# Kernel optimization log

Measured on AMD Instinct MI355X. Metric: run time of the kernel, lower is better.

## Reference

```python
import jax, jax.numpy as jnp
import numpy as np

HEAD_DIM = 64
N_HEADS = 12
ROPE_BASE = 10000.0


def _rope_tables(seq_len, head_dim, dtype=jnp.float32):
    half = head_dim // 2
    inv_freq = 1.0 / (ROPE_BASE ** (jnp.arange(0, half, dtype=jnp.float32) / half))
    pos = jnp.arange(seq_len, dtype=jnp.float32)
    freqs = pos[:, None] * inv_freq[None, :]  # (s, half)
    return jnp.cos(freqs).astype(dtype), jnp.sin(freqs).astype(dtype)


def _apply_rope(t, cos, sin):
    # t: (b, h, s, d); rotate-half convention on full head_dim (rope_fraction=1.0)
    d = t.shape[-1]
    t1, t2 = t[..., : d // 2], t[..., d // 2 :]
    cos = cos[None, None, :, :]
    sin = sin[None, None, :, :]
    return jnp.concatenate([t1 * cos - t2 * sin, t1 * sin + t2 * cos], axis=-1)


def setup_inputs() -> dict:
    key = jax.random.key(0)
    ks = jax.random.split(key, 6)
    b, s, d_model = 16, 512, 768
    x = jax.random.normal(ks[0], (b, s, d_model), dtype=jnp.float32)
    chain_ids = jax.random.randint(ks[1], (b, s), 0, 2, dtype=jnp.int32)
    attention_mask = jnp.ones((b, s), dtype=bool)
    inner = N_HEADS * HEAD_DIM
    scale = 0.02
    Wq = jax.random.normal(ks[2], (d_model, inner), dtype=jnp.float32) * scale
    Wk = jax.random.normal(ks[3], (d_model, inner), dtype=jnp.float32) * scale
    Wv = jax.random.normal(ks[4], (d_model, inner), dtype=jnp.float32) * scale
    Wo = jax.random.normal(ks[5], (inner, d_model), dtype=jnp.float32) * scale
    return {"x": x, "chain_ids": chain_ids, "attention_mask": attention_mask,
            "Wq": Wq, "Wk": Wk, "Wv": Wv, "Wo": Wo}


def reference(x, chain_ids, attention_mask, Wq, Wk, Wv, Wo):
    b, s, _ = x.shape
    h, d = N_HEADS, HEAD_DIM
    scale = d ** (-0.5)

    def proj(W):
        return jnp.einsum('bse,ef->bsf', x, W).reshape(b, s, h, d).transpose(0, 2, 1, 3)

    q = proj(Wq)  # (b, h, s, d)
    k = proj(Wk)
    v = proj(Wv)

    cos, sin = _rope_tables(s, d, x.dtype)
    q_rope = _apply_rope(q, cos, sin)
    k_rope = _apply_rope(k, cos, sin)

    scores_intra = jnp.einsum('bhsd,bhtd->bhst', q_rope, k_rope) * scale
    scores_inter = jnp.einsum('bhsd,bhtd->bhst', q, k) * scale

    # intra-chain mask (b, 1, s, s)
    intra = (chain_ids[:, None, :, None] == chain_ids[:, None, None, :])
    merged = jnp.where(intra, scores_intra, scores_inter)

    # additive padding mask (b, 1, 1, s)
    pad = jnp.where(attention_mask[:, None, None, :], 0.0, -jnp.inf).astype(x.dtype)
    merged = merged + pad

    attn = jax.nn.softmax(merged, axis=-1)
    attn = jnp.nan_to_num(attn, nan=0.0)

    out = jnp.einsum('bhst,bhtd->bhsd', attn, v)
    out = out.transpose(0, 2, 1, 3).reshape(b, s, h * d)
    return jnp.einsum('bsf,fe->bse', out, Wo)
```

## Files before the change

kernel.cpp:

```cpp
#include <hip/hip_runtime.h>
#include <stdint.h>
#include <math.h>

#define NB 16
#define NS 512
#define NH 12
#define ND 64
#define NE 768
#define NF 768

typedef __attribute__((ext_vector_type(4))) float  f32x4;
typedef __attribute__((ext_vector_type(8))) short  bf16x8;
typedef __attribute__((ext_vector_type(4))) short  bf16x4;

#define AS1(p) ((const __attribute__((address_space(1))) unsigned int*)(p))
#define AS3(p) ((__attribute__((address_space(3))) unsigned int*)(p))

__device__ __forceinline__ short f2bf(float f) {
    unsigned u = __builtin_bit_cast(unsigned, f);
    u += 0x7FFFu + ((u >> 16) & 1u);
    return (short)(u >> 16);
}
__device__ __forceinline__ float bf2f(short s) {
    unsigned u = ((unsigned)(unsigned short)s) << 16;
    return __builtin_bit_cast(float, u);
}
__device__ __forceinline__ unsigned pkbf2(float a, float b) {
    return (unsigned)(unsigned short)f2bf(a) | ((unsigned)(unsigned short)f2bf(b) << 16);
}

#define MFMA16(a, b, c) __builtin_amdgcn_mfma_f32_16x16x32_bf16((a), (b), (c), 0, 0, 0)

__device__ __forceinline__ bf16x8 lds_rd8(const short* base, int row, int cb) {
    return *(const bf16x8*)((const char*)base + (((row) * 128 + (cb)) ^ (((row) & 7) << 4)));
}

__global__ __launch_bounds__(256) void prep_kernel(float* __restrict__ cos_t,
                                                   float* __restrict__ sin_t,
                                                   const unsigned char* __restrict__ m,
                                                   int* __restrict__ flag) {
    if (blockIdx.x == 64) {
        __shared__ int any;
        if (threadIdx.x == 0) any = 0;
        __syncthreads();
        int acc = 0;
        for (int i = threadIdx.x; i < NB * NS; i += 256)
            if ((i & 3) && m[i]) acc = 1;
        if (acc) atomicOr(&any, 1);
        __syncthreads();
        if (threadIdx.x == 0) *flag = any;
        return;
    }
    int i = blockIdx.x * 256 + threadIdx.x;
    int p = i >> 5, j = i & 31;
    float inv_freq = powf(10000.0f, -(float)j / 32.0f);
    float ang = (float)p * inv_freq;
    cos_t[i] = cosf(ang);
    sin_t[i] = sinf(ang);
}

__global__ __launch_bounds__(256) void convert_x_kernel(const float* __restrict__ x,
                                                        short* __restrict__ xb) {
    int i = (blockIdx.x * 256 + threadIdx.x) * 8;
    if (i >= 8192 * 768) return;
    float4 a = *(const float4*)&x[i];
    float4 b = *(const float4*)&x[i + 4];
    bf16x8 r = { f2bf(a.x), f2bf(a.y), f2bf(a.z), f2bf(a.w),
                 f2bf(b.x), f2bf(b.y), f2bf(b.z), f2bf(b.w) };
    *(bf16x8*)&xb[i] = r;
}

__global__ __launch_bounds__(256) void convert_wt_kernel(
    const float* __restrict__ Wq, const float* __restrict__ Wk,
    const float* __restrict__ Wv, const float* __restrict__ Wo,
    short* __restrict__ Wqt, short* __restrict__ Wkt,
    short* __restrict__ Wvt, short* __restrict__ Wot) {
    const float* W  = (blockIdx.z == 0) ? Wq  : (blockIdx.z == 1) ? Wk  : (blockIdx.z == 2) ? Wv  : Wo;
    short*       Wt = (blockIdx.z == 0) ? Wqt : (blockIdx.z == 1) ? Wkt : (blockIdx.z == 2) ? Wvt : Wot;
    const int k0 = blockIdx.y * 64, n0 = blockIdx.x * 64;
    __shared__ float t[64][65];
    for (int u = threadIdx.x; u < 4096; u += 256) {
        int r = u >> 6, c = u & 63;
        t[r][c] = W[(size_t)(k0 + r) * 768 + n0 + c];
    }
    __syncthreads();
    for (int u = threadIdx.x; u < 4096; u += 256) {
        int c = u >> 6, r = u & 63;
        Wt[(size_t)(n0 + c) * 768 + k0 + r] = f2bf(t[r][c]);
    }
}

__global__ __launch_bounds__(256) void gemm_qkv_kernel(const short* __restrict__ xb,
    const short* __restrict__ Wqt, const short* __restrict__ Wkt, const short* __restrict__ Wvt,
    short* __restrict__ qo, short* __restrict__ ko, short* __restrict__ vto) {
    const int z = blockIdx.z;
    const short* Bt = (z == 0) ? Wqt : (z == 1) ? Wkt : Wvt;
    short*       O  = (z == 0) ? qo  : (z == 1) ? ko  : vto;
    const int n0 = blockIdx.x * 128, m0 = blockIdx.y * 128;
    __shared__ short As[128 * 64], Bs[128 * 64];
    const int tid = threadIdx.x, lane = tid & 63, wave = tid >> 6;
    const int g = lane >> 4, l15 = lane & 15;
    const int wm = wave >> 1, wn = wave & 1;
    f32x4 acc[4][4];
    #pragma unroll
    for (int i = 0; i < 4; ++i)
        #pragma unroll
        for (int j = 0; j < 4; ++j) acc[i][j] = (f32x4){0.f, 0.f, 0.f, 0.f};

    for (int kt = 0; kt < 12; ++kt) {
        __syncthreads();
        const char* Asrc = (const char*)(xb + (size_t)m0 * 768 + kt * 64);
        const char* Bsrc = (const char*)(Bt + (size_t)n0 * 768 + kt * 64);
        #pragma unroll
        for (int p = 0; p < 4; ++p) {
            int dstoff = (wave * 4 + p) * 1024;
            int off = dstoff + lane * 16;
            int row = off >> 7, slot = off & 127;
            int srcs = slot ^ ((row & 7) << 4);
            __builtin_amdgcn_global_load_lds(AS1(Asrc + (size_t)row * 1536 + srcs),
                                             AS3((char*)As + dstoff), 16, 0, 0);
            __builtin_amdgcn_global_load_lds(AS1(Bsrc + (size_t)row * 1536 + srcs),
                                             AS3((char*)Bs + dstoff), 16, 0, 0);
        }
        __syncthreads();
        __builtin_amdgcn_s_setprio(1);
        #pragma unroll
        for (int h2 = 0; h2 < 2; ++h2) {
            bf16x8 af[4], bfr[4];
            const int cb = h2 * 64 + g * 16;
            #pragma unroll
            for (int i = 0; i < 4; ++i) {
                af[i]  = lds_rd8(As, wm * 64 + i * 16 + l15, cb);
                bfr[i] = lds_rd8(Bs, wn * 64 + i * 16 + l15, cb);
            }
            #pragma unroll
            for (int i = 0; i < 4; ++i)
                #pragma unroll
                for (int j = 0; j < 4; ++j)
                    acc[i][j] = MFMA16(af[i], bfr[j], acc[i][j]);
        }
        __builtin_amdgcn_s_setprio(0);
    }
    #pragma unroll
    for (int i = 0; i < 4; ++i)
        #pragma unroll
        for (int r = 0; r < 4; ++r) {
            int mm = m0 + wm * 64 + i * 16 + g * 4 + r;
            int bb = mm >> 9, ss = mm & 511;
            #pragma unroll
            for (int j = 0; j < 4; ++j) {
                int n = n0 + wn * 64 + j * 16 + l15;
                int hh = n >> 6, dd = n & 63;
                short val = f2bf(acc[i][j][r]);
                if (z == 2)
                    O[(((size_t)bb * NH + hh) * ND + dd) * NS + ss] = val;
                else
                    O[(((size_t)bb * NH + hh) * NS + ss) * ND + dd] = val;
            }
        }
}

__global__ __launch_bounds__(256) void attn_fused_kernel(
    const short* __restrict__ qr, const short* __restrict__ kr, const short* __restrict__ vt,
    const float* __restrict__ cos_t, const float* __restrict__ sin_t,
    const int* __restrict__ chain, const void* __restrict__ amask,
    const int* __restrict__ mflag, short* __restrict__ aout) {
    const int lid = blockIdx.x;
    const int xcd = lid & 7, idx = lid >> 3;
    const int qt = idx & 7, bhl = idx >> 3;
    const int bh = xcd * 24 + bhl;
    const int b = bh / 12, h = bh - (bh / 12) * 12;
    const int q0 = qt * 64;

    __shared__ short Kr_s[4096];
    __shared__ short Kp_s[4096];
    __shared__ short Vt_s[4096];
    __shared__ __align__(16) int   ck_s[64];
    __shared__ __align__(16) float kb_s[64];

    const int tid = threadIdx.x, lane = tid & 63, wave = tid >> 6;
    const int g = lane >> 4, l15 = lane & 15;
    const int m_u8 = *mflag;
    const size_t bhNS = (size_t)bh * NS;
    const float SC = 0.18033688011f;

    const short* qrs = qr + (bhNS + q0) * ND;
    #pragma unroll
    for (int p = 0; p < 2; ++p) {
        int u = tid + p * 256;
        int row = u >> 3, slot = u & 7;
        int off = (row * 128 + slot * 16) ^ ((row & 7) << 4);
        *(bf16x8*)((char*)Kr_s + off) = *(const bf16x8*)(qrs + row * 64 + slot * 8);
    }
    __syncthreads();
    const int qrow = wave * 16 + l15;
    bf16x8 fqr0 = lds_rd8(Kr_s, qrow, g * 16);
    bf16x8 fqr1 = lds_rd8(Kr_s, qrow, 64 + g * 16);
    bf16x8 fqp0, fqp1;
    {
        int pos = q0 + qrow;
        float4 c0 = *(const float4*)&cos_t[pos * 32 + g * 8];
        float4 c1 = *(const float4*)&cos_t[pos * 32 + g * 8 + 4];
        float4 s0 = *(const float4*)&sin_t[pos * 32 + g * 8];
        float4 s1 = *(const float4*)&sin_t[pos * 32 + g * 8 + 4];
        float cc[8] = {c0.x, c0.y, c0.z, c0.w, c1.x, c1.y, c1.z, c1.w};
        float ss[8] = {s0.x, s0.y, s0.z, s0.w, s1.x, s1.y, s1.z, s1.w};
        #pragma unroll
        for (int j = 0; j < 8; ++j) {
            float t1 = bf2f(fqr0[j]), t2 = bf2f(fqr1[j]);
            fqp0[j] = f2bf(t1 * cc[j] - t2 * ss[j]);
            fqp1[j] = f2bf(t1 * ss[j] + t2 * cc[j]);
        }
    }
    const int cqv = chain[b * NS + q0 + qrow];

    float m_run = -INFINITY, l_run = 0.f;
    f32x4 accO[4];
    #pragma unroll
    for (int t = 0; t < 4; ++t) accO[t] = (f32x4){0.f, 0.f, 0.f, 0.f};

    const short* krb = kr + bhNS * ND;
    const char*  vtb = (const char*)(vt + bhNS * ND);

    for (int kv = 0; kv < 8; ++kv) {
        const int k0s = kv * 64;
        __syncthreads();
        {
            int key = tid >> 2, d8 = (tid & 3) * 8;
            const short* krow = krb + (k0s + key) * 64;
            bf16x8 lo = *(const bf16x8*)(krow + d8);
            bf16x8 hi = *(const bf16x8*)(krow + 32 + d8);
            float4 c0 = *(const float4*)&cos_t[(k0s + key) * 32 + d8];
            float4 c1 = *(const float4*)&cos_t[(k0s + key) * 32 + d8 + 4];
            float4 s0 = *(const float4*)&sin_t[(k0s + key) * 32 + d8];
            float4 s1 = *(const float4*)&sin_t[(k0s + key) * 32 + d8 + 4];
            float cc[8] = {c0.x, c0.y, c0.z, c0.w, c1.x, c1.y, c1.z, c1.w};
            float ss[8] = {s0.x, s0.y, s0.z, s0.w, s1.x, s1.y, s1.z, s1.w};
            bf16x8 plo, phi;
            #pragma unroll
            for (int j = 0; j < 8; ++j) {
                float t1 = bf2f(lo[j]), t2 = bf2f(hi[j]);
                plo[j] = f2bf(t1 * cc[j] - t2 * ss[j]);
                phi[j] = f2bf(t1 * ss[j] + t2 * cc[j]);
            }
            int basebyte = key * 128 + d8 * 2;
            int sw = (key & 7) << 4;
            *(bf16x8*)((char*)Kr_s + ((basebyte) ^ sw))      = lo;
            *(bf16x8*)((char*)Kr_s + ((basebyte + 64) ^ sw)) = hi;
            *(bf16x8*)((char*)Kp_s + ((basebyte) ^ sw))      = plo;
            *(bf16x8*)((char*)Kp_s + ((basebyte + 64) ^ sw)) = phi;
        }
        #pragma unroll
        for (int p = 0; p < 2; ++p) {
            int dstoff = (wave * 2 + p) * 1024;
            int off = dstoff + lane * 16;
            int d = off >> 7, slot = off & 127;
            int srcs = slot ^ ((d & 7) << 4);
            __builtin_amdgcn_global_load_lds(AS1(vtb + (size_t)d * 1024 + k0s * 2 + srcs),
                                             AS3((char*)Vt_s + dstoff), 16, 0, 0);
        }
        if (tid < 64) {
            int gidx = b * NS + k0s + tid;
            ck_s[tid] = chain[gidx];
            int ok = m_u8 ? (int)((const unsigned char*)amask)[gidx] : ((const int*)amask)[gidx];
            kb_s[tid] = ok ? 0.f : -INFINITY;
        }
        __syncthreads();

        float pm[4][4];
        float tm = -INFINITY;
        __builtin_amdgcn_s_setprio(1);
        #pragma unroll
        for (int t = 0; t < 4; ++t) {
            bf16x8 akr0 = lds_rd8(Kr_s, t * 16 + l15, g * 16);
            bf16x8 akr1 = lds_rd8(Kr_s, t * 16 + l15, 64 + g * 16);
            bf16x8 akp0 = lds_rd8(Kp_s, t * 16 + l15, g * 16);
            bf16x8 akp1 = lds_rd8(Kp_s, t * 16 + l15, 64 + g * 16);
            f32x4 sr = (f32x4){0.f, 0.f, 0.f, 0.f};
            f32x4 sp = (f32x4){0.f, 0.f, 0.f, 0.f};
            sr = MFMA16(akr0, fqr0, sr);
            sr = MFMA16(akr1, fqr1, sr);
            sp = MFMA16(akp0, fqp0, sp);
            sp = MFMA16(akp1, fqp1, sp);
            int4   ck4 = *(const int4*)&ck_s[t * 16 + g * 4];
            float4 kb4 = *(const float4*)&kb_s[t * 16 + g * 4];
            const int   ckk[4] = {ck4.x, ck4.y, ck4.z, ck4.w};
            const float kbb[4] = {kb4.x, kb4.y, kb4.z, kb4.w};
            #pragma unroll
            for (int r = 0; r < 4; ++r) {
                float sv = (cqv == ckk[r]) ? sp[r] : sr[r];
                sv = sv * SC + kbb[r];
                pm[t][r] = sv;
                tm = fmaxf(tm, sv);
            }
        }
        __builtin_amdgcn_s_setprio(0);
        __syncthreads();

        tm = fmaxf(tm, __shfl_xor(tm, 16));
        tm = fmaxf(tm, __shfl_xor(tm, 32));
        bool skip = __all(tm - m_run <= 8.f);
        float mnew, fac;
        if (skip) { mnew = m_run; fac = 1.f; }
        else      { mnew = fmaxf(m_run, tm); fac = exp2f(m_run - mnew); }
        float psum = 0.f;
        if (mnew == -INFINITY) {
            #pragma unroll
            for (int t = 0; t < 4; ++t)
                #pragma unroll
                for (int r = 0; r < 4; ++r) pm[t][r] = 0.f;
            fac = 1.f;
        } else {
            #pragma unroll
            for (int t = 0; t < 4; ++t)
                #pragma unroll
                for (int r = 0; r < 4; ++r) {
                    float p = exp2f(pm[t][r] - mnew);
                    pm[t][r] = p;
                    psum += p;
                }
        }
        psum += __shfl_xor(psum, 16);
        psum += __shfl_xor(psum, 32);
        l_run = l_run * fac + psum;
        m_run = mnew;

        char* pwave = (char*)Kr_s + wave * 2048;
        int psw = (l15 & 7) << 4;
        #pragma unroll
        for (int t = 0; t < 4; ++t) {
            unsigned u0 = pkbf2(pm[t][0], pm[t][1]);
            unsigned u1 = pkbf2(pm[t][2], pm[t][3]);
            uint2 pk = {u0, u1};
            *(uint2*)(pwave + ((l15 * 128 + t * 32 + g * 8) ^ psw)) = pk;
        }
        if (!skip) {
            float f4[4];
            #pragma unroll
            for (int r = 0; r < 4; ++r) f4[r] = __shfl(fac, g * 4 + r);
            #pragma unroll
            for (int t = 0; t < 4; ++t) {
                f32x4 a = accO[t];
                a[0] *= f4[0]; a[1] *= f4[1]; a[2] *= f4[2]; a[3] *= f4[3];
                accO[t] = a;
            }
        }
        bf16x8 pa0 = *(const bf16x8*)(pwave + ((l15 * 128 + g * 16) ^ psw));
        bf16x8 pa1 = *(const bf16x8*)(pwave + ((l15 * 128 + 64 + g * 16) ^ psw));
        __builtin_amdgcn_s_setprio(1);
        #pragma unroll
        for (int dt = 0; dt < 4; ++dt) {
            bf16x8 vb0 = lds_rd8(Vt_s, dt * 16 + l15, g * 16);
            bf16x8 vb1 = lds_rd8(Vt_s, dt * 16 + l15, 64 + g * 16);
            accO[dt] = MFMA16(pa0, vb0, accO[dt]);
            accO[dt] = MFMA16(pa1, vb1, accO[dt]);
        }
        __builtin_amdgcn_s_setprio(0);
    }

    float inv[4];
    #pragma unroll
    for (int r = 0; r < 4; ++r) {
        float lv = __shfl(l_run, g * 4 + r);
        inv[r] = (lv > 0.f) ? 1.f / lv : 0.f;
    }
    #pragma unroll
    for (int dt = 0; dt < 4; ++dt)
        #pragma unroll
        for (int r = 0; r < 4; ++r) {
            int row = b * NS + q0 + wave * 16 + g * 4 + r;
            aout[(size_t)row * NF + h * ND + dt * 16 + l15] = f2bf(accO[dt][r] * inv[r]);
        }
}

__global__ __launch_bounds__(256) void gemm_out_kernel(const short* __restrict__ A,
    const short* __restrict__ Wot, float* __restrict__ out) {
    const int n0 = blockIdx.x * 128, m0 = blockIdx.y * 64;
    __shared__ short As[64 * 64], Bs[128 * 64];
    const int tid = threadIdx.x, lane = tid & 63, wave = tid >> 6;
    const int g = lane >> 4, l15 = lane & 15;
    const int wm = wave >> 1, wn = wave & 1;
    f32x4 acc[2][4];
    #pragma unroll
    for (int i = 0; i < 2; ++i)
        #pragma unroll
        for (int j = 0; j < 4; ++j) acc[i][j] = (f32x4){0.f, 0.f, 0.f, 0.f};

    for (int kt = 0; kt < 12; ++kt) {
        __syncthreads();
        const char* Asrc = (const char*)(A   + (size_t)m0 * 768 + kt * 64);
        const char* Bsrc = (const char*)(Wot + (size_t)n0 * 768 + kt * 64);
        #pragma unroll
        for (int p = 0; p < 2; ++p) {
            int dstoff = (wave * 2 + p) * 1024;
            int off = dstoff + lane * 16;
            int row = off >> 7, slot = off & 127;
            int srcs = slot ^ ((row & 7) << 4);
            __builtin_amdgcn_global_load_lds(AS1(Asrc + (size_t)row * 1536 + srcs),
                                             AS3((char*)As + dstoff), 16, 0, 0);
        }
        #pragma unroll
        for (int p = 0; p < 4; ++p) {
            int dstoff = (wave * 4 + p) * 1024;
            int off = dstoff + lane * 16;
            int row = off >> 7, slot = off & 127;
            int srcs = slot ^ ((row & 7) << 4);
            __builtin_amdgcn_global_load_lds(AS1(Bsrc + (size_t)row * 1536 + srcs),
                                             AS3((char*)Bs + dstoff), 16, 0, 0);
        }
        __syncthreads();
        __builtin_amdgcn_s_setprio(1);
        #pragma unroll
        for (int h2 = 0; h2 < 2; ++h2) {
            bf16x8 af[2], bfr[4];
            const int cb = h2 * 64 + g * 16;
            #pragma unroll
            for (int i = 0; i < 2; ++i)
                af[i]  = lds_rd8(As, wm * 32 + i * 16 + l15, cb);
            #pragma unroll
            for (int j = 0; j < 4; ++j)
                bfr[j] = lds_rd8(Bs, wn * 64 + j * 16 + l15, cb);
            #pragma unroll
            for (int i = 0; i < 2; ++i)
                #pragma unroll
                for (int j = 0; j < 4; ++j)
                    acc[i][j] = MFMA16(af[i], bfr[j], acc[i][j]);
        }
        __builtin_amdgcn_s_setprio(0);
    }
    #pragma unroll
    for (int i = 0; i < 2; ++i)
        #pragma unroll
        for (int r = 0; r < 4; ++r) {
            int mm = m0 + wm * 32 + i * 16 + g * 4 + r;
            #pragma unroll
            for (int j = 0; j < 4; ++j) {
                int n = n0 + wn * 64 + j * 16 + l15;
                out[(size_t)mm * NE + n] = acc[i][j][r];
            }
        }
}

extern "C" void kernel_launch(void* const* d_in, const int* in_sizes, int n_in,
                              void* d_out, int out_size, void* d_ws, size_t ws_size,
                              hipStream_t stream) {
    const float* x     = (const float*)d_in[0];
    const int*   chain = (const int*)d_in[1];
    const void*  amask = d_in[2];
    const float* Wq = (const float*)d_in[3];
    const float* Wk = (const float*)d_in[4];
    const float* Wv = (const float*)d_in[5];
    const float* Wo = (const float*)d_in[6];
    float* out = (float*)d_out;

    const size_t QSZ = (size_t)NB * NH * NS * ND;
    char* w = (char*)d_ws;
    float* cos_t = (float*)w;  w += (size_t)NS * 32 * 4;
    float* sin_t = (float*)w;  w += (size_t)NS * 32 * 4;
    int*   mflag = (int*)w;    w += 256;
    short* xb    = (short*)w;  w += (size_t)8192 * 768 * 2;
    short* Wqt   = (short*)w;  w += (size_t)768 * 768 * 2;
    short* Wkt   = (short*)w;  w += (size_t)768 * 768 * 2;
    short* Wvt   = (short*)w;  w += (size_t)768 * 768 * 2;
    short* Wot   = (short*)w;  w += (size_t)768 * 768 * 2;
    short* q_raw = (short*)w;  w += QSZ * 2;
    short* k_raw = (short*)w;  w += QSZ * 2;
    short* vtr   = (short*)w;  w += QSZ * 2;
    short* aout  = xb;

    prep_kernel<<<dim3(65), dim3(256), 0, stream>>>(cos_t, sin_t,
                                                    (const unsigned char*)amask, mflag);
    convert_x_kernel<<<dim3(3072), dim3(256), 0, stream>>>(x, xb);
    convert_wt_kernel<<<dim3(12, 12, 4), dim3(256), 0, stream>>>(Wq, Wk, Wv, Wo, Wqt, Wkt, Wvt, Wot);
    gemm_qkv_kernel<<<dim3(6, 64, 3), dim3(256), 0, stream>>>(xb, Wqt, Wkt, Wvt, q_raw, k_raw, vtr);
    attn_fused_kernel<<<dim3(1536), dim3(256), 0, stream>>>(q_raw, k_raw, vtr, cos_t, sin_t,
                                                            chain, amask, mflag, aout);
    gemm_out_kernel<<<dim3(6, 128), dim3(256), 0, stream>>>(aout, Wot, out);
}
```

Before: 159.8 us.

## Precompute rotated K in QKV GEMM epilogue and stream K tiles via async LDS loads

The QKV GEMM epilogue now also writes a RoPE-rotated copy of K, so the attention kernel no longer rotates K for every query tile. In the attention kernel, raw K, rotated K and V tiles are loaded with global_load_lds, and chain ids and padding bias for the whole sequence are staged once. A separate P buffer lets one barrier per KV step be dropped. The cost is an extra K-sized global write and read, plus more shared memory per block, which may lower occupancy.

After: 166.7 us. 1.04x slower.

```diff
diff --git a/kernel.cpp b/kernel.cpp
--- a/kernel.cpp
+++ b/kernel.cpp
@@ -92,7 +92,9 @@
 
 __global__ __launch_bounds__(256) void gemm_qkv_kernel(const short* __restrict__ xb,
     const short* __restrict__ Wqt, const short* __restrict__ Wkt, const short* __restrict__ Wvt,
-    short* __restrict__ qo, short* __restrict__ ko, short* __restrict__ vto) {
+    const float* __restrict__ cos_t, const float* __restrict__ sin_t,
+    short* __restrict__ qo, short* __restrict__ ko, short* __restrict__ kpo,
+    short* __restrict__ vto) {
     const int z = blockIdx.z;
     const short* Bt = (z == 0) ? Wqt : (z == 1) ? Wkt : Wvt;
     short*       O  = (z == 0) ? qo  : (z == 1) ? ko  : vto;
@@ -141,27 +143,41 @@
         }
         __builtin_amdgcn_s_setprio(0);
     }
+    const int hh = (n0 + wn * 64) >> 6;
     #pragma unroll
     for (int i = 0; i < 4; ++i)
         #pragma unroll
         for (int r = 0; r < 4; ++r) {
             int mm = m0 + wm * 64 + i * 16 + g * 4 + r;
             int bb = mm >> 9, ss = mm & 511;
-            #pragma unroll
-            for (int j = 0; j < 4; ++j) {
-                int n = n0 + wn * 64 + j * 16 + l15;
-                int hh = n >> 6, dd = n & 63;
-                short val = f2bf(acc[i][j][r]);
-                if (z == 2)
-                    O[(((size_t)bb * NH + hh) * ND + dd) * NS + ss] = val;
-                else
-                    O[(((size_t)bb * NH + hh) * NS + ss) * ND + dd] = val;
+            if (z == 2) {
+                #pragma unroll
+                for (int j = 0; j < 4; ++j) {
+                    int dd = j * 16 + l15;
+                    O[(((size_t)bb * NH + hh) * ND + dd) * NS + ss] = f2bf(acc[i][j][r]);
+                }
+            } else {
+                size_t base = (((size_t)bb * NH + hh) * NS + ss) * ND;
+                #pragma unroll
+                for (int j = 0; j < 4; ++j)
+                    O[base + j * 16 + l15] = f2bf(acc[i][j][r]);
+                if (z == 1) {
+                    #pragma unroll
+                    for (int p2 = 0; p2 < 2; ++p2) {
+                        int jf = p2 * 16 + l15;
+                        float c = cos_t[ss * 32 + jf], s = sin_t[ss * 32 + jf];
+                        float t1 = acc[i][p2][r], t2 = acc[i][p2 + 2][r];
+                        kpo[base + jf]      = f2bf(t1 * c - t2 * s);
+                        kpo[base + 32 + jf] = f2bf(t1 * s + t2 * c);
+                    }
+                }
             }
         }
 }
 
 __global__ __launch_bounds__(256) void attn_fused_kernel(
-    const short* __restrict__ qr, const short* __restrict__ kr, const short* __restrict__ vt,
+    const short* __restrict__ qr, const short* __restrict__ kr, const short* __restrict__ kp,
+    const short* __restrict__ vt,
     const float* __restrict__ cos_t, const float* __restrict__ sin_t,
     const int* __restrict__ chain, const void* __restrict__ amask,
     const int* __restrict__ mflag, short* __restrict__ aout) {
@@ -175,8 +191,9 @@
     __shared__ short Kr_s[4096];
     __shared__ short Kp_s[4096];
     __shared__ short Vt_s[4096];
-    __shared__ __align__(16) int   ck_s[64];
-    __shared__ __align__(16) float kb_s[64];
+    __shared__ short P_s[4096];
+    __shared__ int   ck_a[512];
+    __shared__ float kb_a[512];
 
     const int tid = threadIdx.x, lane = tid & 63, wave = tid >> 6;
     const int g = lane >> 4, l15 = lane & 15;
@@ -184,13 +201,21 @@
     const size_t bhNS = (size_t)bh * NS;
     const float SC = 0.18033688011f;
 
-    const short* qrs = qr + (bhNS + q0) * ND;
+    for (int u = tid; u < NS; u += 256) {
+        int gidx = b * NS + u;
+        ck_a[u] = chain[gidx];
+        int ok = m_u8 ? (int)((const unsigned char*)amask)[gidx] : ((const int*)amask)[gidx];
+        kb_a[u] = ok ? 0.f : -INFINITY;
+    }
+    const char* qrsC = (const char*)(qr + (bhNS + q0) * ND);
     #pragma unroll
     for (int p = 0; p < 2; ++p) {
-        int u = tid + p * 256;
-        int row = u >> 3, slot = u & 7;
-        int off = (row * 128 + slot * 16) ^ ((row & 7) << 4);
-        *(bf16x8*)((char*)Kr_s + off) = *(const bf16x8*)(qrs + row * 64 + slot * 8);
+        int dstoff = (wave * 2 + p) * 1024;
+        int off = dstoff + lane * 16;
+        int row = off >> 7, slot = off & 127;
+        int srcs = slot ^ ((row & 7) << 4);
+        __builtin_amdgcn_global_load_lds(AS1(qrsC + (size_t)row * 128 + srcs),
+                                         AS3((char*)Kr_s + dstoff), 16, 0, 0);
     }
     __syncthreads();
     const int qrow = wave * 16 + l15;
@@ -212,58 +237,31 @@
             fqp1[j] = f2bf(t1 * ss[j] + t2 * cc[j]);
         }
     }
-    const int cqv = chain[b * NS + q0 + qrow];
+    const int cqv = ck_a[q0 + qrow];
 
     float m_run = -INFINITY, l_run = 0.f;
     f32x4 accO[4];
     #pragma unroll
     for (int t = 0; t < 4; ++t) accO[t] = (f32x4){0.f, 0.f, 0.f, 0.f};
 
-    const short* krb = kr + bhNS * ND;
-    const char*  vtb = (const char*)(vt + bhNS * ND);
+    const char* krC = (const char*)(kr + bhNS * ND);
+    const char* kpC = (const char*)(kp + bhNS * ND);
+    const char* vtC = (const char*)(vt + bhNS * ND);
 
     for (int kv = 0; kv < 8; ++kv) {
         const int k0s = kv * 64;
         __syncthreads();
-        {
-            int key = tid >> 2, d8 = (tid & 3) * 8;
-            const short* krow = krb + (k0s + key) * 64;
-            bf16x8 lo = *(const bf16x8*)(krow + d8);
-            bf16x8 hi = *(const bf16x8*)(krow + 32 + d8);
-            float4 c0 = *(const float4*)&cos_t[(k0s + key) * 32 + d8];
-            float4 c1 = *(const float4*)&cos_t[(k0s + key) * 32 + d8 + 4];
-            float4 s0 = *(const float4*)&sin_t[(k0s + key) * 32 + d8];
-            float4 s1 = *(const float4*)&sin_t[(k0s + key) * 32 + d8 + 4];
-            float cc[8] = {c0.x, c0.y, c0.z, c0.w, c1.x, c1.y, c1.z, c1.w};
-            float ss[8] = {s0.x, s0.y, s0.z, s0.w, s1.x, s1.y, s1.z, s1.w};
-            bf16x8 plo, phi;
-            #pragma unroll
-            for (int j = 0; j < 8; ++j) {
-                float t1 = bf2f(lo[j]), t2 = bf2f(hi[j]);
-                plo[j] = f2bf(t1 * cc[j] - t2 * ss[j]);
-                phi[j] = f2bf(t1 * ss[j] + t2 * cc[j]);
-            }
-            int basebyte = key * 128 + d8 * 2;
-            int sw = (key & 7) << 4;
-            *(bf16x8*)((char*)Kr_s + ((basebyte) ^ sw))      = lo;
-            *(bf16x8*)((char*)Kr_s + ((basebyte + 64) ^ sw)) = hi;
-            *(bf16x8*)((char*)Kp_s + ((basebyte) ^ sw))      = plo;
-            *(bf16x8*)((char*)Kp_s + ((basebyte + 64) ^ sw)) = phi;
-        }
         #pragma unroll
         for (int p = 0; p < 2; ++p) {
             int dstoff = (wave * 2 + p) * 1024;
             int off = dstoff + lane * 16;
-            int d = off >> 7, slot = off & 127;
-            int srcs = slot ^ ((d & 7) << 4);
-            __builtin_amdgcn_global_load_lds(AS1(vtb + (size_t)d * 1024 + k0s * 2 + srcs),
+            int row = off >> 7, slot = off & 127;
+            int srcs = slot ^ ((row & 7) << 4);
+            size_t koff = (size_t)(k0s + row) * 128 + srcs;
+            __builtin_amdgcn_global_load_lds(AS1(krC + koff), AS3((char*)Kr_s + dstoff), 16, 0, 0);
+            __builtin_amdgcn_global_load_lds(AS1(kpC + koff), AS3((char*)Kp_s + dstoff), 16, 0, 0);
+            __builtin_amdgcn_global_load_lds(AS1(vtC + (size_t)row * 1024 + k0s * 2 + srcs),
                                              AS3((char*)Vt_s + dstoff), 16, 0, 0);
-        }
-        if (tid < 64) {
-            int gidx = b * NS + k0s + tid;
-            ck_s[tid] = chain[gidx];
-            int ok = m_u8 ? (int)((const unsigned char*)amask)[gidx] : ((const int*)amask)[gidx];
-            kb_s[tid] = ok ? 0.f : -INFINITY;
         }
         __syncthreads();
 
@@ -282,8 +280,8 @@
             sr = MFMA16(akr1, fqr1, sr);
             sp = MFMA16(akp0, fqp0, sp);
             sp = MFMA16(akp1, fqp1, sp);
-            int4   ck4 = *(const int4*)&ck_s[t * 16 + g * 4];
-            float4 kb4 = *(const float4*)&kb_s[t * 16 + g * 4];
+            int4   ck4 = *(const int4*)&ck_a[k0s + t * 16 + g * 4];
+            float4 kb4 = *(const float4*)&kb_a[k0s + t * 16 + g * 4];
             const int   ckk[4] = {ck4.x, ck4.y, ck4.z, ck4.w};
             const float kbb[4] = {kb4.x, kb4.y, kb4.z, kb4.w};
             #pragma unroll
@@ -295,7 +293,6 @@
             }
         }
         __builtin_amdgcn_s_setprio(0);
-        __syncthreads();
 
         tm = fmaxf(tm, __shfl_xor(tm, 16));
         tm = fmaxf(tm, __shfl_xor(tm, 32));
@@ -325,7 +322,7 @@
         l_run = l_run * fac + psum;
         m_run = mnew;
 
-        char* pwave = (char*)Kr_s + wave * 2048;
+        char* pwave = (char*)P_s + wave * 2048;
         int psw = (l15 & 7) << 4;
         #pragma unroll
         for (int t = 0; t < 4; ++t) {
@@ -465,6 +462,7 @@
     short* Wot   = (short*)w;  w += (size_t)768 * 768 * 2;
     short* q_raw = (short*)w;  w += QSZ * 2;
     short* k_raw = (short*)w;  w += QSZ * 2;
+    short* k_rop = (short*)w;  w += QSZ * 2;
     short* vtr   = (short*)w;  w += QSZ * 2;
     short* aout  = xb;
 
@@ -472,8 +470,9 @@
                                                     (const unsigned char*)amask, mflag);
     convert_x_kernel<<<dim3(3072), dim3(256), 0, stream>>>(x, xb);
     convert_wt_kernel<<<dim3(12, 12, 4), dim3(256), 0, stream>>>(Wq, Wk, Wv, Wo, Wqt, Wkt, Wvt, Wot);
-    gemm_qkv_kernel<<<dim3(6, 64, 3), dim3(256), 0, stream>>>(xb, Wqt, Wkt, Wvt, q_raw, k_raw, vtr);
-    attn_fused_kernel<<<dim3(1536), dim3(256), 0, stream>>>(q_raw, k_raw, vtr, cos_t, sin_t,
-                                                            chain, amask, mflag, aout);
+    gemm_qkv_kernel<<<dim3(6, 64, 3), dim3(256), 0, stream>>>(xb, Wqt, Wkt, Wvt, cos_t, sin_t,
+                                                              q_raw, k_raw, k_rop, vtr);
+    attn_fused_kernel<<<dim3(1536), dim3(256), 0, stream>>>(q_raw, k_raw, k_rop, vtr,
+                                                            cos_t, sin_t, chain, amask, mflag, aout);
     gemm_out_kernel<<<dim3(6, 128), dim3(256), 0, stream>>>(aout, Wot, out);
 }
```
